# Kernel optimization log

Measured on AMD Instinct MI355X. Metric: run time of the kernel, lower is better.

The kernel has to match this reference:

```python
import jax, jax.numpy as jnp
import numpy as np

HEADS = 8
DIM_HEAD_KQ = 8
DIM_HEAD_V = 16
DIM = 128
IN_CH = 128
QKV_CH = DIM_HEAD_V + 2 * DIM_HEAD_KQ  # 32
OUT_CH = HEADS * QKV_CH               # 256
EPS = 1e-5


def setup_inputs() -> dict:
    key = jax.random.key(0)
    ks = jax.random.split(key, 7)
    b = 2048  # batch * width
    return {
        "x_in": jax.random.normal(ks[0], (b, IN_CH, DIM), jnp.float32),
        "conv_w": jax.random.normal(ks[1], (OUT_CH, IN_CH), jnp.float32) * (IN_CH ** -0.5),
        "bn_gamma": 1.0 + 0.1 * jax.random.normal(ks[2], (OUT_CH,), jnp.float32),
        "bn_beta": 0.1 * jax.random.normal(ks[3], (OUT_CH,), jnp.float32),
        "bn_mean": 0.1 * jax.random.normal(ks[4], (OUT_CH,), jnp.float32),
        "bn_var": jax.random.uniform(ks[5], (OUT_CH,), jnp.float32, 0.5, 1.5),
        "relative": jax.random.normal(ks[6], (QKV_CH, 2 * DIM - 1), jnp.float32),
    }


def reference(x_in, conv_w, bn_gamma, bn_beta, bn_mean, bn_var, relative):
    scale = DIM ** -0.5
    b = x_in.shape[0]

    # 1x1 conv + BatchNorm1d (inference mode, running stats)
    y = jnp.einsum('bcd,oc->bod', x_in, conv_w)  # [b, 256, DIM]
    inv = bn_gamma / jnp.sqrt(bn_var + EPS)
    y = (y - bn_mean[:, None]) * inv[:, None] + bn_beta[:, None]

    # rearrange 'b (q h) d -> b h q d' with q=QKV_CH, h=HEADS
    qkv = y.reshape(b, QKV_CH, HEADS, DIM).transpose(0, 2, 1, 3)  # [b,h,32,DIM]
    q = qkv[:, :, :DIM_HEAD_KQ] * scale           # [b,h,8,DIM]
    k = qkv[:, :, DIM_HEAD_KQ:2 * DIM_HEAD_KQ]    # [b,h,8,DIM]
    v = qkv[:, :, 2 * DIM_HEAD_KQ:]               # [b,h,16,DIM]

    # relative position gather: all_emb[c, a, j] = relative[c, a - j + DIM - 1]
    idx = jnp.arange(DIM)
    rel_idx = idx[:, None] - idx[None, :] + DIM - 1  # [DIM, DIM]
    all_emb = relative[:, rel_idx]                   # [32, DIM, DIM]
    q_emb = all_emb[:DIM_HEAD_KQ]
    k_emb = all_emb[DIM_HEAD_KQ:2 * DIM_HEAD_KQ]
    v_emb = all_emb[2 * DIM_HEAD_KQ:]

    qr = jnp.einsum('bhid,idj->bhdj', q, q_emb)      # [b,h,DIM,DIM]
    kr = jnp.einsum('bhid,idj->bhdj', k, k_emb)
    dots = jnp.einsum('bhid,bhij->bhdj', q, k)
    attn = jax.nn.softmax(qr + kr + dots, axis=-1)

    out = jnp.einsum('bhdj,bhij->bhid', attn, v)     # [b,h,16,DIM]
    kv = jnp.einsum('bhdj,idj->bhid', attn, v_emb)   # [b,h,16,DIM]

    # rearrange 'b h i d -> b (h i) d'
    return (kv + out).reshape(b, HEADS * DIM_HEAD_V, DIM)
```

## Files before the change

### kernel.cpp

```cpp
#include <hip/hip_runtime.h>

typedef __attribute__((ext_vector_type(8))) short short8;
typedef __attribute__((ext_vector_type(4))) short short4v;
typedef __attribute__((ext_vector_type(4))) float float4v;
typedef unsigned short ushort_t;
typedef __bf16 bf16_t;

#define MFMA16(A,B,C) __builtin_amdgcn_mfma_f32_16x16x32_bf16((A),(B),(C),0,0,0)
#define LOG2E 1.4426950408889634f

#define WS_BYTES 29440

#define OFF_EQKH 0
#define OFF_EQKL 10240
#define OFF_WH   20480
#define OFF_WL   29184
#define OFF_QH   20480
#define OFF_QL   26624
#define OFF_ATT  0
#define OFF_EVR  37888
#define OFF_V    46848
#define OFF_IB   51200
#define LDS_BYTES 51456

__device__ __forceinline__ ushort_t f2bf(float f) {
  return __builtin_bit_cast(ushort_t, (bf16_t)f);
}
__device__ __forceinline__ float bf2f(ushort_t s) {
  return __builtin_bit_cast(float, ((unsigned)s) << 16);
}
__device__ __forceinline__ short8 ld8_2x4(const char* p) {
  short4v a = *(const short4v*)p;
  short4v b = *(const short4v*)(p + 8);
  return (short8){a[0],a[1],a[2],a[3],b[0],b[1],b[2],b[3]};
}
__device__ __forceinline__ short8 sel8(bool c, short8 a) {
  short8 r;
  #pragma unroll
  for (int k = 0; k < 8; ++k) r[k] = c ? a[k] : (short)0;
  return r;
}

__global__ __launch_bounds__(512) void prep_rel(const float* __restrict__ relg,
                                                char* __restrict__ ws) {
  int idx = blockIdx.x * 512 + threadIdx.x;
  if (idx < 4096) {
    int i = idx & 15, t = idx >> 4;
    float r1 = 0.f;
    if (t < 255) r1 = relg[i * 255 + (254 - t)] * LOG2E;
    ushort_t h1 = f2bf(r1);
    *(ushort_t*)(ws + t * 40 + i * 2)         = h1;
    *(ushort_t*)(ws + 10240 + t * 40 + i * 2) = f2bf(r1 - bf2f(h1));
  } else if (idx < 8576) {
    int k = idx - 4096;
    int i = k / 280, c = k - i * 280;
    float r2 = 0.f;
    if (c < 255) r2 = relg[(16 + i) * 255 + (254 - c)];
    *(ushort_t*)(ws + 20480 + i * 560 + c * 2) = f2bf(r2);
  }
}

__global__ __launch_bounds__(512, 6) void axial_fused(
    const float* __restrict__ xg,
    const float* __restrict__ wg,
    const float* __restrict__ gg, const float* __restrict__ btg,
    const float* __restrict__ mng, const float* __restrict__ vrg,
    const char* __restrict__ wsg,
    float* __restrict__ outg)
{
  __shared__ __align__(64) char L[LDS_BYTES];
  const int tid  = threadIdx.x;
  const unsigned bid = blockIdx.x;
  const int xcd = bid & 7;
  const unsigned li = bid >> 3;
  const int h = (int)(li & 7);
  const int b = (int)((li >> 3) * 8 + (unsigned)xcd);
  const int w    = tid >> 6;
  const int lane = tid & 63;
  const int q    = lane >> 4;
  const int m16  = lane & 15;
  const int qbase = lane & 48;

  #pragma unroll
  for (int u0 = 0; u0 < 1280; u0 += 512) {
    int u = u0 + tid;
    if (u < 1280) *(float4v*)(L + u * 16) = *(const float4v*)(wsg + u * 16);
  }
  {
    *(float4v*)(L + OFF_EVR + tid * 16) = *(const float4v*)(wsg + 20480 + tid * 16);
    if (tid < 48) {
      int u2 = 512 + tid;
      *(float4v*)(L + OFF_EVR + u2 * 16) = *(const float4v*)(wsg + 20480 + u2 * 16);
    }
  }
  {
    int o = tid >> 4, c0 = (tid & 15) * 8;
    const float* wrow = wg + (o * 8 + h) * 128 + c0;
    short8 hi, lo;
    #pragma unroll
    for (int k = 0; k < 8; ++k) {
      float f = wrow[k];
      ushort_t hh = f2bf(f);
      hi[k] = (short)hh; lo[k] = (short)f2bf(f - bf2f(hh));
    }
    *(short8*)(L + OFF_WH + o * 272 + c0 * 2) = hi;
    *(short8*)(L + OFF_WL + o * 272 + c0 * 2) = lo;
  }
  if (tid < 32) {
    int og = tid * 8 + h;
    float inv = gg[og] / sqrtf(vrg[og] + 1e-5f);
    ((float*)(L + OFF_IB))[tid * 2]     = inv;
    ((float*)(L + OFF_IB))[tid * 2 + 1] = btg[og] - mng[og] * inv;
  }
  __syncthreads();

  float4v acc0 = {0,0,0,0}, acc1 = {0,0,0,0};
  {
    const int d = w * 16 + m16;
    const float* xb = xg + (size_t)b * 16384 + d;
    #pragma unroll
    for (int cc = 0; cc < 4; ++cc) {
      const int cb = cc * 32;
      short8 xh, xl;
      #pragma unroll
      for (int jj = 0; jj < 8; ++jj) {
        float xv = xb[(cb + q * 8 + jj) * 128];
        ushort_t hh = f2bf(xv);
        xh[jj] = (short)hh; xl[jj] = (short)f2bf(xv - bf2f(hh));
      }
      const char* wbh = L + OFF_WH + m16 * 272 + (cb + q * 8) * 2;
      const char* wbl = L + OFF_WL + m16 * 272 + (cb + q * 8) * 2;
      short8 wh0 = *(const short8*)(wbh);
      short8 wh1 = *(const short8*)(wbh + 16 * 272);
      short8 wl0 = *(const short8*)(wbl);
      short8 wl1 = *(const short8*)(wbl + 16 * 272);
      acc0 = MFMA16(wh0, xh, acc0);
      acc0 = MFMA16(wl0, xh, acc0);
      acc0 = MFMA16(wh0, xl, acc0);
      acc1 = MFMA16(wh1, xh, acc1);
      acc1 = MFMA16(wl1, xh, acc1);
      acc1 = MFMA16(wh1, xl, acc1);
    }
  }
  __syncthreads();

  {
    const int d = w * 16 + m16;
    const float* ib = (const float*)(L + OFF_IB);
    {
      const float sc = (q < 2) ? 0.08838834764831845f : 1.0f;
      short4v hi4, lo4, kt4;
      #pragma unroll
      for (int r = 0; r < 4; ++r) {
        int o = q * 4 + r;
        float y = (acc0[r] * ib[o * 2] + ib[o * 2 + 1]) * sc;
        ushort_t hh = f2bf(y);
        hi4[r] = (short)hh; lo4[r] = (short)f2bf(y - bf2f(hh));
        kt4[r] = (short)f2bf(y * LOG2E);
      }
      *(short4v*)(L + OFF_QH + d * 48 + q * 8) = hi4;
      *(short4v*)(L + OFF_QL + d * 40 + q * 8) = lo4;
      if (q >= 2) *(short4v*)(L + OFF_QH + d * 48 + 32 + (q - 2) * 8) = kt4;
    }
    #pragma unroll
    for (int r = 0; r < 4; ++r) {
      int o = 16 + q * 4 + r;
      float y = acc1[r] * ib[o * 2] + ib[o * 2 + 1];
      *(ushort_t*)(L + OFF_V + (q * 4 + r) * 272 + d * 2) = f2bf(y);
    }
  }
  __syncthreads();

  const int toff = 112 - w * 16;
  const int rowd = w * 16 + m16;
  short8 A1 = *(const short8*)(L + OFF_QH + rowd * 48 + (q & 1) * 16);
  short8 A2 = sel8(q < 2, ld8_2x4(L + OFF_QL + rowd * 40 + (q & 1) * 16));
  float4v sc[9];
  {
    const char* eb = L + ((q < 2) ? OFF_EQKH : OFF_EQKL) + (q & 1) * 16;
    #pragma unroll
    for (int tk = 0; tk < 9; ++tk) {
      short8 b1 = ld8_2x4(eb + (tk * 16 + m16 + toff) * 40);
      float4v z = {0,0,0,0};
      float4v c = MFMA16(A1, b1, z);
      sc[tk] = MFMA16(A2, b1, c);
    }
  }
  {
    short8 Ad = sel8(q == 0, A1);
    const int base0 = m16 + q * 4 + 1;
    #pragma unroll
    for (int jt = 0; jt < 8; ++jt) {
      short8 bk = *(const short8*)(L + OFF_QH + (jt * 16 + m16) * 48 + 32);
      float4v z = {0,0,0,0};
      float4v c = MFMA16(Ad, bk, z);
      #pragma unroll
      for (int r = 0; r < 4; ++r) {
        int u = base0 + r;
        int sl = (u & 15) | qbase;
        float rot = __shfl(c[r], sl, 64);
        bool ge = (u & 16) != 0;
        sc[jt][r]     += ge ? rot : 0.0f;
        sc[jt + 1][r] += ge ? 0.0f : rot;
      }
    }
    #pragma unroll
    for (int r = 0; r < 4; ++r) {
      bool ge = ((base0 + r) & 16) != 0;
      sc[0][r] = ge ? sc[0][r] : -1e30f;
      sc[8][r] = ge ? -1e30f : sc[8][r];
    }
  }
  __syncthreads();

  float rs[4];
  {
    #pragma unroll
    for (int r = 0; r < 4; ++r) {
      float mx = sc[0][r];
      #pragma unroll
      for (int tk = 1; tk < 9; ++tk) mx = fmaxf(mx, sc[tk][r]);
      #pragma unroll
      for (int off = 1; off <= 8; off <<= 1) mx = fmaxf(mx, __shfl_xor(mx, off, 64));
      float e[9]; float s = 0.f;
      #pragma unroll
      for (int tk = 0; tk < 9; ++tk) { e[tk] = __builtin_exp2f(sc[tk][r] - mx); s += e[tk]; }
      #pragma unroll
      for (int off = 1; off <= 8; off <<= 1) s += __shfl_xor(s, off, 64);
      rs[r] = 1.0f / s;
      const int dd = w * 16 + q * 4 + r;
      const size_t rowp = (size_t)(L + OFF_ATT) + (size_t)dd * 288;
      const size_t sw = ((dd >> 2) & 3) << 4;
      #pragma unroll
      for (int tk = 0; tk < 9; ++tk)
        *(ushort_t*)((rowp + (tk * 16 + m16) * 2) ^ sw) = f2bf(e[tk]);
    }
  }
  __syncthreads();

  {
    float4v acc = {0,0,0,0};
    const char* evrow = L + OFF_EVR + m16 * 560;
    const char* vrow  = L + OFF_V + m16 * 272;
    const size_t abase = (size_t)(L + OFF_ATT) + (size_t)rowd * 288;
    const size_t swz = ((rowd >> 2) & 3) << 4;
    #pragma unroll
    for (int kk = 0; kk < 4; ++kk) {
      short8 af;
      #pragma unroll
      for (int jj = 0; jj < 8; ++jj) {
        int ttg = kk * 32 + q * 8 + jj + 15 - m16;
        af[jj] = *(const short*)((abase + ttg * 2) ^ swz);
      }
      short8 bf = *(const short8*)(vrow + (kk * 32 + q * 8) * 2);
      acc = MFMA16(af, bf, acc);
    }
    #pragma unroll
    for (int kk = 0; kk < 5; ++kk) {
      short8 af;
      if (kk == 4 && q >= 2) af = (short8){0,0,0,0,0,0,0,0};
      else af = *(const short8*)((abase + (kk * 32 + q * 8) * 2) ^ swz);
      short8 bf = *(const short8*)(evrow + (toff + kk * 32 + q * 8) * 2);
      acc = MFMA16(af, bf, acc);
    }
    #pragma unroll
    for (int r = 0; r < 4; ++r) acc[r] *= rs[r];
    float* op = outg + (size_t)b * 16384 + (h * 16 + m16) * 128 + w * 16 + q * 4;
    *(float4v*)op = acc;
  }
}

extern "C" void kernel_launch(void* const* d_in, const int* in_sizes, int n_in,
                              void* d_out, int out_size, void* d_ws, size_t ws_size,
                              hipStream_t stream) {
  const float* xg   = (const float*)d_in[0];
  const float* wg   = (const float*)d_in[1];
  const float* gg   = (const float*)d_in[2];
  const float* btg  = (const float*)d_in[3];
  const float* mng  = (const float*)d_in[4];
  const float* vrg  = (const float*)d_in[5];
  const float* relg = (const float*)d_in[6];
  float* outg = (float*)d_out;
  char* ws = (char*)d_ws;
  prep_rel<<<dim3(17), dim3(512), 0, stream>>>(relg, ws);
  axial_fused<<<dim3(16384), dim3(512), 0, stream>>>(xg, wg, gg, btg, mng, vrg, ws, outg);
}
```

Measured before the change: 487.1 us.

## Drop softmax max-subtraction and compute row sums via MFMA with ones

Removes the per-row max reduction (shuffles) and subtracts no max before exp2, relying on bounded logits. Boundary masking becomes a multiply by 0/1 masks instead of -1e30 selects. Row sums are produced by extra MFMAs against a ones vector using the bf16-rounded attention weights, replacing the shuffle-based sum reduction and using a fast reciprocal. This risks overflow for large scores and adds 5 MFMAs per wave.

```diff
diff --git a/kernel.cpp b/kernel.cpp
--- a/kernel.cpp
+++ b/kernel.cpp
@@ -186,9 +186,16 @@
       sc[tk] = MFMA16(A2, b1, c);
     }
   }
-  {
+  float mk[4], mkb[4];
+  {
+    const int base0 = m16 + q * 4 + 1;
+    #pragma unroll
+    for (int r = 0; r < 4; ++r) {
+      bool ge = ((base0 + r) & 16) != 0;
+      mk[r]  = ge ? 1.0f : 0.0f;
+      mkb[r] = 1.0f - mk[r];
+    }
     short8 Ad = sel8(q == 0, A1);
-    const int base0 = m16 + q * 4 + 1;
     #pragma unroll
     for (int jt = 0; jt < 8; ++jt) {
       short8 bk = *(const short8*)(L + OFF_QH + (jt * 16 + m16) * 48 + 32);
@@ -196,38 +203,23 @@
       float4v c = MFMA16(Ad, bk, z);
       #pragma unroll
       for (int r = 0; r < 4; ++r) {
-        int u = base0 + r;
-        int sl = (u & 15) | qbase;
+        int sl = ((base0 + r) & 15) | qbase;
         float rot = __shfl(c[r], sl, 64);
-        bool ge = (u & 16) != 0;
-        sc[jt][r]     += ge ? rot : 0.0f;
-        sc[jt + 1][r] += ge ? 0.0f : rot;
-      }
-    }
+        sc[jt][r]     += rot * mk[r];
+        sc[jt + 1][r] += rot * mkb[r];
+      }
+    }
+  }
+  __syncthreads();
+
+  {
     #pragma unroll
     for (int r = 0; r < 4; ++r) {
-      bool ge = ((base0 + r) & 16) != 0;
-      sc[0][r] = ge ? sc[0][r] : -1e30f;
-      sc[8][r] = ge ? -1e30f : sc[8][r];
-    }
-  }
-  __syncthreads();
-
-  float rs[4];
-  {
-    #pragma unroll
-    for (int r = 0; r < 4; ++r) {
-      float mx = sc[0][r];
-      #pragma unroll
-      for (int tk = 1; tk < 9; ++tk) mx = fmaxf(mx, sc[tk][r]);
-      #pragma unroll
-      for (int off = 1; off <= 8; off <<= 1) mx = fmaxf(mx, __shfl_xor(mx, off, 64));
-      float e[9]; float s = 0.f;
-      #pragma unroll
-      for (int tk = 0; tk < 9; ++tk) { e[tk] = __builtin_exp2f(sc[tk][r] - mx); s += e[tk]; }
-      #pragma unroll
-      for (int off = 1; off <= 8; off <<= 1) s += __shfl_xor(s, off, 64);
-      rs[r] = 1.0f / s;
+      float e[9];
+      #pragma unroll
+      for (int tk = 0; tk < 9; ++tk) e[tk] = __builtin_exp2f(sc[tk][r]);
+      e[0] *= mk[r];
+      e[8] *= mkb[r];
       const int dd = w * 16 + q * 4 + r;
       const size_t rowp = (size_t)(L + OFF_ATT) + (size_t)dd * 288;
       const size_t sw = ((dd >> 2) & 3) << 4;
@@ -239,7 +231,9 @@
   __syncthreads();
 
   {
-    float4v acc = {0,0,0,0};
+    float4v acc  = {0,0,0,0};
+    float4v accs = {0,0,0,0};
+    const short8 ones = {16256,16256,16256,16256,16256,16256,16256,16256};
     const char* evrow = L + OFF_EVR + m16 * 560;
     const char* vrow  = L + OFF_V + m16 * 272;
     const size_t abase = (size_t)(L + OFF_ATT) + (size_t)rowd * 288;
@@ -261,10 +255,12 @@
       if (kk == 4 && q >= 2) af = (short8){0,0,0,0,0,0,0,0};
       else af = *(const short8*)((abase + (kk * 32 + q * 8) * 2) ^ swz);
       short8 bf = *(const short8*)(evrow + (toff + kk * 32 + q * 8) * 2);
-      acc = MFMA16(af, bf, acc);
-    }
-    #pragma unroll
-    for (int r = 0; r < 4; ++r) acc[r] *= rs[r];
+      acc  = MFMA16(af, bf, acc);
+      accs = MFMA16(af, ones, accs);
+    }
+    #pragma unroll
+    for (int r = 0; r < 4; ++r)
+      acc[r] *= __builtin_amdgcn_rcpf(accs[r]);
     float* op = outg + (size_t)b * 16384 + (h * 16 + m16) * 128 + w * 16 + q * 4;
     *(float4v*)op = acc;
   }
```

Result: no change. 496.5 us (+1.9%).
